# Optimization experiments

Measured on AMD Instinct MI355X. Metric: run time of the kernel, lower is better.

Reference implementation:

```python
import jax, jax.numpy as jnp
import numpy as np

B, V, NF, K = 16, 5000, 352, 120


def setup_inputs() -> dict:
    key = jax.random.key(0)
    k1, k2, k3, k4 = jax.random.split(key, 4)
    return {
        "feat_x": jax.random.normal(k1, (B, V, NF), dtype=jnp.float32),
        "feat_y": jax.random.normal(k2, (B, V, NF), dtype=jnp.float32),
        "evecs_x": jax.random.normal(k3, (B, V, K), dtype=jnp.float32),
        "evecs_y": jax.random.normal(k4, (B, V, K), dtype=jnp.float32),
    }


def reference(feat_x, feat_y, evecs_x, evecs_y):
    # Spectral coefficients: F_hat[b] = (evecs_x[b]^T feat_x[b])^T -> [B, F, K]
    F_hat = jnp.einsum("bvk,bvf->bfk", evecs_x, feat_x)
    G_hat = jnp.einsum("bvk,bvf->bfk", evecs_y, feat_y)

    # C1[b] = (inv(F^T F) F^T G)^T, batched least-squares solve
    FtF = jnp.einsum("bfk,bfl->bkl", F_hat, F_hat)  # [B,K,K]
    FtG = jnp.einsum("bfk,bfl->bkl", F_hat, G_hat)  # [B,K,K]
    C1 = jnp.linalg.solve(FtF, FtG).transpose(0, 2, 1)

    GtG = jnp.einsum("bfk,bfl->bkl", G_hat, G_hat)
    GtF = jnp.einsum("bfk,bfl->bkl", G_hat, F_hat)
    C2 = jnp.linalg.solve(GtG, GtF).transpose(0, 2, 1)
    return (C1, C2)
```

## Files before the change

### kernel.cpp

```cpp
#include <hip/hip_runtime.h>
#include <hip/hip_bf16.h>

#define NB 16
#define VV 5000
#define NFD 352
#define KD 120

typedef __attribute__((ext_vector_type(8))) short short8;
typedef __attribute__((ext_vector_type(4))) float float4v;

__device__ __forceinline__ void load_lds16(const float* g, float* l) {
    __builtin_amdgcn_global_load_lds(
        (const __attribute__((address_space(1))) unsigned int*)g,
        (__attribute__((address_space(3))) unsigned int*)l, 16, 0, 0);
}

__device__ __forceinline__ short bfbits(const __hip_bfloat16 h) {
    return (short)__builtin_bit_cast(unsigned short, h);
}

template <int STRIDE>
__device__ __forceinline__ void cvt_frag(const float* p, short8& hi, short8& lo) {
    #pragma unroll
    for (int j = 0; j < 8; ++j) {
        const float a = p[j * STRIDE];
        const __hip_bfloat16 h = __float2bfloat16(a);
        const float hf = __bfloat162float(h);
        const __hip_bfloat16 l = __float2bfloat16(a - hf);
        hi[j] = bfbits(h);
        lo[j] = bfbits(l);
    }
}

__global__ __launch_bounds__(256, 2) void proj_mfma(
    const float* __restrict__ fx, const float* __restrict__ fy,
    const float* __restrict__ ex, const float* __restrict__ ey,
    float* __restrict__ partials, const float* __restrict__ zeropad)
{
    const int t  = threadIdx.x;
    const int mt = blockIdx.x & 3;
    const int ch = blockIdx.x >> 2;
    const int wh = blockIdx.y;
    const int b  = blockIdx.z;

    const float* Ab = (wh ? fy : fx) + (size_t)b * VV * NFD;
    const float* Bb = (wh ? ey : ex) + (size_t)b * VV * KD;
    const int m0 = mt * 96;

    __shared__ float ldsA[64 * 96];
    __shared__ float ldsB[64 * 128];

    int akk[6]; const float* asrc0[6]; bool aok[6];
    #pragma unroll
    for (int i = 0; i < 6; ++i) {
        const int e  = i * 1024 + t * 4;
        const int k  = e / 96;
        const int c4 = (e - k * 96) >> 2;
        const int s  = ((k >> 3) & 3) << 1;
        const int mg = c4 ^ s;
        const int col = m0 + (mg << 2);
        akk[i] = k;
        aok[i] = (col < NFD);
        asrc0[i] = Ab + col;
    }
    int bkk[8]; const float* bsrc0[8]; bool bok[8];
    #pragma unroll
    for (int i = 0; i < 8; ++i) {
        const int e  = i * 1024 + t * 4;
        const int k  = e >> 7;
        const int c4 = (e >> 2) & 31;
        const int s  = ((k >> 3) & 3) << 1;
        const int ng = c4 ^ s;
        const int col = ng << 2;
        bkk[i] = k;
        bok[i] = (col < KD);
        bsrc0[i] = Bb + col;
    }

    const int wid = t >> 6;
    const int lane = t & 63;
    const int wm = wid >> 1, wn = wid & 1;
    const int row16 = lane & 15;
    const int g = lane >> 4;
    const int sl = (g & 3) << 1;

    int aidx[3];
    #pragma unroll
    for (int mf = 0; mf < 3; ++mf) {
        const int m = wm * 48 + mf * 16 + row16;
        aidx[mf] = (g * 8) * 96 + ((((m >> 2) ^ sl)) << 2) + (m & 3);
    }
    int bidx[4];
    #pragma unroll
    for (int nf = 0; nf < 4; ++nf) {
        const int n = wn * 64 + nf * 16 + row16;
        bidx[nf] = (g * 8) * 128 + ((((n >> 2) ^ sl)) << 2) + (n & 3);
    }

    float4v acc[3][4];
    #pragma unroll
    for (int mf = 0; mf < 3; ++mf)
        #pragma unroll
        for (int nf = 0; nf < 4; ++nf)
            acc[mf][nf] = float4v{0.f, 0.f, 0.f, 0.f};

    const int step0  = ch * 20;
    const int nsteps = (ch < 3) ? 20 : 19;

    for (int st = 0; st < nsteps; ++st) {
        const int v0 = (step0 + st) * 64;

        #pragma unroll
        for (int i = 0; i < 6; ++i) {
            const int v = v0 + akk[i];
            const float* src = (aok[i] && v < VV) ? (asrc0[i] + (size_t)v * NFD) : zeropad;
            load_lds16(src, &ldsA[i * 1024 + t * 4]);
        }
        #pragma unroll
        for (int i = 0; i < 8; ++i) {
            const int v = v0 + bkk[i];
            const float* src = (bok[i] && v < VV) ? (bsrc0[i] + (size_t)v * KD) : zeropad;
            load_lds16(src, &ldsB[i * 1024 + t * 4]);
        }
        __syncthreads();

        #pragma unroll
        for (int ks = 0; ks < 2; ++ks) {
            short8 ah[3], al[3], bh[4], bl[4];
            #pragma unroll
            for (int mf = 0; mf < 3; ++mf)
                cvt_frag<96>(&ldsA[ks * 32 * 96 + aidx[mf]], ah[mf], al[mf]);
            #pragma unroll
            for (int nf = 0; nf < 4; ++nf)
                cvt_frag<128>(&ldsB[ks * 32 * 128 + bidx[nf]], bh[nf], bl[nf]);

            #pragma unroll
            for (int mf = 0; mf < 3; ++mf)
                #pragma unroll
                for (int nf = 0; nf < 4; ++nf) {
                    acc[mf][nf] = __builtin_amdgcn_mfma_f32_16x16x32_bf16(ah[mf], bh[nf], acc[mf][nf], 0, 0, 0);
                    acc[mf][nf] = __builtin_amdgcn_mfma_f32_16x16x32_bf16(ah[mf], bl[nf], acc[mf][nf], 0, 0, 0);
                    acc[mf][nf] = __builtin_amdgcn_mfma_f32_16x16x32_bf16(al[mf], bh[nf], acc[mf][nf], 0, 0, 0);
                }
        }
        __syncthreads();
    }

    float* slab = partials + (size_t)((ch * 2 + wh) * NB + b) * (352 * 128);
    #pragma unroll
    for (int mf = 0; mf < 3; ++mf) {
        const int mrow = mt * 96 + wm * 48 + mf * 16 + g * 4;
        #pragma unroll
        for (int nf = 0; nf < 4; ++nf) {
            const int n = wn * 64 + nf * 16 + row16;
            #pragma unroll
            for (int r = 0; r < 4; ++r) {
                const int m = mrow + r;
                if (m < NFD) slab[(size_t)m * 128 + n] = acc[mf][nf][r];
            }
        }
    }
}

__global__ __launch_bounds__(256) void reduce_k(
    const float* __restrict__ partials, float* __restrict__ fhat, float* __restrict__ ghat)
{
    const int id = blockIdx.x * 256 + threadIdx.x;
    if (id >= NFD * KD) return;
    const int wb = blockIdx.y;
    const int wh = wb >> 4;
    const int b  = wb & 15;
    const int f = id / KD;
    const int k = id - f * KD;

    const size_t slabsz = 352 * 128;
    const float* p = partials + (size_t)(wh * NB + b) * slabsz + (size_t)f * 128 + k;
    const size_t chstride = (size_t)2 * NB * slabsz;

    float s = 0.f;
    #pragma unroll
    for (int c = 0; c < 4; ++c) s += p[c * chstride];

    float* dst = (wh ? ghat : fhat) + (size_t)b * NFD * KD + id;
    *dst = s;
}

__device__ __forceinline__ void gemm_tn_64x64(
    const float* __restrict__ A, const float* __restrict__ B, float* __restrict__ C,
    int V, int M, int N, int m0, int n0)
{
    __shared__ float As[16][64];
    __shared__ float Bs[16][64];

    const int tid = threadIdx.x;
    const int tx = tid & 15;
    const int ty = tid >> 4;
    const int sr = tid >> 4;
    const int sc = (tid & 15) << 2;

    float acc[4][4] = {{0.f,0.f,0.f,0.f},{0.f,0.f,0.f,0.f},
                       {0.f,0.f,0.f,0.f},{0.f,0.f,0.f,0.f}};

    for (int v0 = 0; v0 < V; v0 += 16) {
        const int v = v0 + sr;
        float4 av; av.x = av.y = av.z = av.w = 0.f;
        float4 bv; bv.x = bv.y = bv.z = bv.w = 0.f;
        if (v < V) {
            const float* Ar = A + (size_t)v * M;
            const int ca = m0 + sc;
            if (ca + 3 < M) {
                av = *(const float4*)(Ar + ca);
            } else {
                if (ca + 0 < M) av.x = Ar[ca + 0];
                if (ca + 1 < M) av.y = Ar[ca + 1];
                if (ca + 2 < M) av.z = Ar[ca + 2];
                if (ca + 3 < M) av.w = Ar[ca + 3];
            }
            const float* Br = B + (size_t)v * N;
            const int cb = n0 + sc;
            if (cb + 3 < N) {
                bv = *(const float4*)(Br + cb);
            } else {
                if (cb + 0 < N) bv.x = Br[cb + 0];
                if (cb + 1 < N) bv.y = Br[cb + 1];
                if (cb + 2 < N) bv.z = Br[cb + 2];
                if (cb + 3 < N) bv.w = Br[cb + 3];
            }
        }
        __syncthreads();
        *(float4*)&As[sr][sc] = av;
        *(float4*)&Bs[sr][sc] = bv;
        __syncthreads();

        #pragma unroll
        for (int kk = 0; kk < 16; ++kk) {
            const float4 a4 = *(const float4*)&As[kk][ty << 2];
            const float4 b4 = *(const float4*)&Bs[kk][tx << 2];
            const float a[4]  = {a4.x, a4.y, a4.z, a4.w};
            const float bb[4] = {b4.x, b4.y, b4.z, b4.w};
            #pragma unroll
            for (int i = 0; i < 4; ++i)
                #pragma unroll
                for (int j = 0; j < 4; ++j)
                    acc[i][j] = fmaf(a[i], bb[j], acc[i][j]);
        }
    }

    #pragma unroll
    for (int i = 0; i < 4; ++i) {
        const int m = m0 + (ty << 2) + i;
        if (m < M) {
            #pragma unroll
            for (int j = 0; j < 4; ++j) {
                const int n = n0 + (tx << 2) + j;
                if (n < N) C[(size_t)m * N + n] = acc[i][j];
            }
        }
    }
}

__global__ __launch_bounds__(256) void gram_kernel(
    const float* __restrict__ fhat, const float* __restrict__ ghat,
    float* __restrict__ ftf, float* __restrict__ gtg, float* __restrict__ ftg)
{
    const int b = blockIdx.z;
    const int which = blockIdx.y;
    const int m0 = (blockIdx.x & 1) * 64;
    const int n0 = (blockIdx.x >> 1) * 64;

    const float* F = fhat + (size_t)b * NFD * KD;
    const float* G = ghat + (size_t)b * NFD * KD;
    const float* A  = (which == 1) ? G : F;
    const float* Bp = (which == 0) ? F : G;
    float* C = ((which == 0) ? ftf : (which == 1) ? gtg : ftg) + (size_t)b * KD * KD;

    gemm_tn_64x64(A, Bp, C, NFD, KD, KD, m0, n0);
}

__device__ __forceinline__ float ldval(const float* __restrict__ A, const float* __restrict__ B,
                                       int pair, int row, int col) {
    if (col < KD) return A[row * KD + col];
    const int l = col - KD;
    return pair ? B[l * KD + row] : B[row * KD + l];
}

#define FOR30(OP) OP(0) OP(1) OP(2) OP(3) OP(4) OP(5) OP(6) OP(7) OP(8) OP(9) \
                  OP(10) OP(11) OP(12) OP(13) OP(14) OP(15) OP(16) OP(17) OP(18) OP(19) \
                  OP(20) OP(21) OP(22) OP(23) OP(24) OP(25) OP(26) OP(27) OP(28) OP(29)

__global__ __launch_bounds__(960, 1) void solve_kernel(
    const float* __restrict__ ftf, const float* __restrict__ gtg,
    const float* __restrict__ ftg, float* __restrict__ out)
{
    const int pair = blockIdx.x;
    const int b = blockIdx.y;
    const int tid = threadIdx.x;
    const int row   = tid >> 3;
    const int cg    = tid & 7;
    const int cbase = cg * 30;

    const float* Ag = ((pair == 0) ? ftf : gtg) + (size_t)b * KD * KD;
    const float* Bg = ftg + (size_t)b * KD * KD;

    __shared__ float prow[2][240];
    __shared__ float pcol[2][120];

    #define DECLC(I) float c##I = ldval(Ag, Bg, pair, row, cbase + (I));
    FOR30(DECLC)
    #undef DECLC

    if (row == 0) {
        #define PUBR0(I) prow[0][cbase + (I)] = c##I;
        FOR30(PUBR0)
        #undef PUBR0
    }
    if (cg == 0) pcol[0][row] = c0;
    __syncthreads();

    for (int j = 0; j < KD; ++j) {
        const int cur = j & 1;
        const int nxt = cur ^ 1;

        const float pinv = 1.0f / prow[cur][j];

        #define PRS(I) const float p##I = prow[cur][cbase + (I)] * pinv;
        FOR30(PRS)
        #undef PRS

        const float f = pcol[cur][row];

        #define UPDC(I) c##I = fmaf(-f, p##I, c##I);
        FOR30(UPDC)
        #undef UPDC

        if (row == j) {
            #define FIXC(I) c##I = p##I;
            FOR30(FIXC)
            #undef FIXC
        }

        const int j2 = j + 1;
        if (row == j2) {
            #define PUBR(I) prow[nxt][cbase + (I)] = c##I;
            FOR30(PUBR)
            #undef PUBR
        }
        if (j2 < KD && cg == (j2 / 30)) {
            #define PCASE(I) case I: pcol[nxt][row] = c##I; break;
            switch (j2 - cbase) {
                FOR30(PCASE)
                default: break;
            }
            #undef PCASE
        }
        __syncthreads();
    }

    float* op = out + (size_t)pair * NB * KD * KD + (size_t)b * KD * KD;
    if (cg >= 4) {
        #define OUTW(I) { const int l = cbase + (I) - KD; op[l * KD + row] = c##I; }
        FOR30(OUTW)
        #undef OUTW
    }
}

extern "C" void kernel_launch(void* const* d_in, const int* in_sizes, int n_in,
                              void* d_out, int out_size, void* d_ws, size_t ws_size,
                              hipStream_t stream)
{
    const float* feat_x  = (const float*)d_in[0];
    const float* feat_y  = (const float*)d_in[1];
    const float* evecs_x = (const float*)d_in[2];
    const float* evecs_y = (const float*)d_in[3];
    float* out = (float*)d_out;

    float* ws       = (float*)d_ws;
    float* zeropad  = ws;
    float* partials = ws + 64;
    float* fhat     = partials + (size_t)4 * 2 * NB * 352 * 128;
    float* ghat     = fhat + (size_t)NB * NFD * KD;
    float* ftf      = ghat + (size_t)NB * NFD * KD;
    float* gtg      = ftf  + (size_t)NB * KD * KD;
    float* ftg      = gtg  + (size_t)NB * KD * KD;

    hipMemsetAsync(zeropad, 0, 256, stream);

    proj_mfma <<<dim3(16, 2, NB), 256, 0, stream>>>(feat_x, feat_y, evecs_x, evecs_y, partials, zeropad);
    reduce_k  <<<dim3(165, 32), 256, 0, stream>>>(partials, fhat, ghat);
    gram_kernel<<<dim3(4, 3, NB), 256, 0, stream>>>(fhat, ghat, ftf, gtg, ftg);
    solve_kernel<<<dim3(2, NB), 960, 0, stream>>>(ftf, gtg, ftg, out);
}
```

Baseline: 250.0 us.

## Register-prefetch projection tiles, pre-split bf16 in LDS, vectorize solve row access

The projection GEMM drops the direct global-to-LDS loads. Each thread now loads into registers, splits the values into bf16 hi/lo once, and stores them swizzled in LDS, with the next tile's loads overlapping the MFMA work on the current tile. The tile grows to 128x128 over 5 V-chunks, and partials are stored compactly with stride 120 so the zero-pad buffer and memset go away. The solve kernel reads and writes pivot rows as float4 and folds pinv into one scalar multiplier. This trades more registers and a larger padded tile (wasted M/N work) for fewer LDS conversions and hidden load latency.

```diff
diff --git a/kernel.cpp b/kernel.cpp
--- a/kernel.cpp
+++ b/kernel.cpp
@@ -5,137 +5,175 @@
 #define VV 5000
 #define NFD 352
 #define KD 120
+#define NCH 5
+#define SLABSZ (352 * 120)
 
 typedef __attribute__((ext_vector_type(8))) short short8;
 typedef __attribute__((ext_vector_type(4))) float float4v;
 
-__device__ __forceinline__ void load_lds16(const float* g, float* l) {
-    __builtin_amdgcn_global_load_lds(
-        (const __attribute__((address_space(1))) unsigned int*)g,
-        (__attribute__((address_space(3))) unsigned int*)l, 16, 0, 0);
-}
-
-__device__ __forceinline__ short bfbits(const __hip_bfloat16 h) {
-    return (short)__builtin_bit_cast(unsigned short, h);
-}
-
-template <int STRIDE>
-__device__ __forceinline__ void cvt_frag(const float* p, short8& hi, short8& lo) {
+__device__ __forceinline__ unsigned short bfb(float a) {
+    return __builtin_bit_cast(unsigned short, __float2bfloat16(a));
+}
+
+__device__ __forceinline__ void pack8(const float* f, int4& hi, int4& lo) {
+    unsigned short h[8], l[8];
     #pragma unroll
     for (int j = 0; j < 8; ++j) {
-        const float a = p[j * STRIDE];
-        const __hip_bfloat16 h = __float2bfloat16(a);
-        const float hf = __bfloat162float(h);
-        const __hip_bfloat16 l = __float2bfloat16(a - hf);
-        hi[j] = bfbits(h);
-        lo[j] = bfbits(l);
-    }
+        const float a = f[j];
+        const __hip_bfloat16 hb = __float2bfloat16(a);
+        h[j] = __builtin_bit_cast(unsigned short, hb);
+        l[j] = bfb(a - __bfloat162float(hb));
+    }
+    hi.x = h[0] | (h[1] << 16); hi.y = h[2] | (h[3] << 16);
+    hi.z = h[4] | (h[5] << 16); hi.w = h[6] | (h[7] << 16);
+    lo.x = l[0] | (l[1] << 16); lo.y = l[2] | (l[3] << 16);
+    lo.z = l[4] | (l[5] << 16); lo.w = l[6] | (l[7] << 16);
 }
 
 __global__ __launch_bounds__(256, 2) void proj_mfma(
     const float* __restrict__ fx, const float* __restrict__ fy,
     const float* __restrict__ ex, const float* __restrict__ ey,
-    float* __restrict__ partials, const float* __restrict__ zeropad)
+    float* __restrict__ partials)
 {
     const int t  = threadIdx.x;
-    const int mt = blockIdx.x & 3;
-    const int ch = blockIdx.x >> 2;
+    const int mt = blockIdx.x % 3;
+    const int ch = blockIdx.x / 3;
     const int wh = blockIdx.y;
     const int b  = blockIdx.z;
 
     const float* Ab = (wh ? fy : fx) + (size_t)b * VV * NFD;
     const float* Bb = (wh ? ey : ex) + (size_t)b * VV * KD;
-    const int m0 = mt * 96;
-
-    __shared__ float ldsA[64 * 96];
-    __shared__ float ldsB[64 * 128];
-
-    int akk[6]; const float* asrc0[6]; bool aok[6];
-    #pragma unroll
-    for (int i = 0; i < 6; ++i) {
-        const int e  = i * 1024 + t * 4;
-        const int k  = e / 96;
-        const int c4 = (e - k * 96) >> 2;
-        const int s  = ((k >> 3) & 3) << 1;
-        const int mg = c4 ^ s;
-        const int col = m0 + (mg << 2);
-        akk[i] = k;
-        aok[i] = (col < NFD);
-        asrc0[i] = Ab + col;
-    }
-    int bkk[8]; const float* bsrc0[8]; bool bok[8];
-    #pragma unroll
-    for (int i = 0; i < 8; ++i) {
-        const int e  = i * 1024 + t * 4;
-        const int k  = e >> 7;
-        const int c4 = (e >> 2) & 31;
-        const int s  = ((k >> 3) & 3) << 1;
-        const int ng = c4 ^ s;
-        const int col = ng << 2;
-        bkk[i] = k;
-        bok[i] = (col < KD);
-        bsrc0[i] = Bb + col;
-    }
-
-    const int wid = t >> 6;
+    const int m0 = mt * 128;
+
+    __shared__ int4 smem4[4096];
+    unsigned char* smem = (unsigned char*)smem4;
+
+    int aoff[4], awb[4], ao[4];
+    #pragma unroll
+    for (int i = 0; i < 4; ++i) {
+        const int q = i * 256 + t;
+        const int m = q & 127;
+        const int o = q >> 7;
+        const int col = min(m0 + m, NFD - 1);
+        aoff[i] = col + o * 8 * NFD;
+        awb[i]  = m * 128 + ((o ^ (m & 7)) * 16);
+        ao[i]   = o;
+    }
+    int boff[4], bwb[4], bo[4];
+    #pragma unroll
+    for (int i = 0; i < 4; ++i) {
+        const int q = i * 256 + t;
+        const int n = q & 127;
+        const int o = q >> 7;
+        const int col = min(n, KD - 1);
+        boff[i] = col + o * 8 * KD;
+        bwb[i]  = 32768 + n * 128 + ((o ^ (n & 7)) * 16);
+        bo[i]   = o;
+    }
+
     const int lane = t & 63;
+    const int wid  = t >> 6;
     const int wm = wid >> 1, wn = wid & 1;
-    const int row16 = lane & 15;
-    const int g = lane >> 4;
-    const int sl = (g & 3) << 1;
-
-    int aidx[3];
-    #pragma unroll
-    for (int mf = 0; mf < 3; ++mf) {
-        const int m = wm * 48 + mf * 16 + row16;
-        aidx[mf] = (g * 8) * 96 + ((((m >> 2) ^ sl)) << 2) + (m & 3);
-    }
-    int bidx[4];
+    const int r16 = lane & 15;
+    const int g   = lane >> 4;
+
+    int abase[4], bbase[4];
+    #pragma unroll
+    for (int mf = 0; mf < 4; ++mf) {
+        const int m = wm * 64 + mf * 16 + r16;
+        abase[mf] = m * 128 + ((g ^ (m & 7)) * 16);
+    }
     #pragma unroll
     for (int nf = 0; nf < 4; ++nf) {
-        const int n = wn * 64 + nf * 16 + row16;
-        bidx[nf] = (g * 8) * 128 + ((((n >> 2) ^ sl)) << 2) + (n & 3);
-    }
-
-    float4v acc[3][4];
-    #pragma unroll
-    for (int mf = 0; mf < 3; ++mf)
+        const int n = wn * 64 + nf * 16 + r16;
+        bbase[nf] = 32768 + n * 128 + ((g ^ (n & 7)) * 16);
+    }
+
+    float4v acc[4][4];
+    #pragma unroll
+    for (int mf = 0; mf < 4; ++mf)
         #pragma unroll
         for (int nf = 0; nf < 4; ++nf)
             acc[mf][nf] = float4v{0.f, 0.f, 0.f, 0.f};
 
-    const int step0  = ch * 20;
-    const int nsteps = (ch < 3) ? 20 : 19;
-
-    for (int st = 0; st < nsteps; ++st) {
-        const int v0 = (step0 + st) * 64;
-
-        #pragma unroll
-        for (int i = 0; i < 6; ++i) {
-            const int v = v0 + akk[i];
-            const float* src = (aok[i] && v < VV) ? (asrc0[i] + (size_t)v * NFD) : zeropad;
-            load_lds16(src, &ldsA[i * 1024 + t * 4]);
-        }
-        #pragma unroll
-        for (int i = 0; i < 8; ++i) {
-            const int v = v0 + bkk[i];
-            const float* src = (bok[i] && v < VV) ? (bsrc0[i] + (size_t)v * KD) : zeropad;
-            load_lds16(src, &ldsB[i * 1024 + t * 4]);
-        }
-        __syncthreads();
+    const int step0 = ch * 16;
+    const int nst   = (ch < 4) ? 16 : 15;
+
+    float fa[4][8], fb[4][8];
+
+    auto do_loads = [&](int v0) {
+        const int va = v0 * NFD;
+        const int vb = v0 * KD;
+        if (v0 + 64 <= VV) {
+            #pragma unroll
+            for (int i = 0; i < 4; ++i)
+                #pragma unroll
+                for (int j = 0; j < 8; ++j)
+                    fa[i][j] = Ab[aoff[i] + va + j * NFD];
+            #pragma unroll
+            for (int i = 0; i < 4; ++i)
+                #pragma unroll
+                for (int j = 0; j < 8; ++j)
+                    fb[i][j] = Bb[boff[i] + vb + j * KD];
+        } else {
+            #pragma unroll
+            for (int i = 0; i < 4; ++i)
+                #pragma unroll
+                for (int j = 0; j < 8; ++j) {
+                    const int v = v0 + ao[i] * 8 + j;
+                    fa[i][j] = (v < VV) ? Ab[aoff[i] + va + j * NFD] : 0.f;
+                }
+            #pragma unroll
+            for (int i = 0; i < 4; ++i)
+                #pragma unroll
+                for (int j = 0; j < 8; ++j) {
+                    const int v = v0 + bo[i] * 8 + j;
+                    fb[i][j] = (v < VV) ? Bb[boff[i] + vb + j * KD] : 0.f;
+                }
+        }
+    };
+    auto do_writes = [&]() {
+        #pragma unroll
+        for (int i = 0; i < 4; ++i) {
+            int4 hi, lo;
+            pack8(fa[i], hi, lo);
+            *(int4*)(smem + awb[i])         = hi;
+            *(int4*)(smem + awb[i] + 16384) = lo;
+        }
+        #pragma unroll
+        for (int i = 0; i < 4; ++i) {
+            int4 hi, lo;
+            pack8(fb[i], hi, lo);
+            *(int4*)(smem + bwb[i])         = hi;
+            *(int4*)(smem + bwb[i] + 16384) = lo;
+        }
+    };
+
+    do_loads(step0 * 64);
+    do_writes();
+    __syncthreads();
+
+    for (int st = 0; st < nst; ++st) {
+        const bool more = (st + 1 < nst);
+        if (more) do_loads((step0 + st + 1) * 64);
 
         #pragma unroll
         for (int ks = 0; ks < 2; ++ks) {
-            short8 ah[3], al[3], bh[4], bl[4];
-            #pragma unroll
-            for (int mf = 0; mf < 3; ++mf)
-                cvt_frag<96>(&ldsA[ks * 32 * 96 + aidx[mf]], ah[mf], al[mf]);
-            #pragma unroll
-            for (int nf = 0; nf < 4; ++nf)
-                cvt_frag<128>(&ldsB[ks * 32 * 128 + bidx[nf]], bh[nf], bl[nf]);
-
-            #pragma unroll
-            for (int mf = 0; mf < 3; ++mf)
+            short8 ah[4], al[4], bh[4], bl[4];
+            #pragma unroll
+            for (int mf = 0; mf < 4; ++mf) {
+                const int ad = abase[mf] ^ (ks * 64);
+                ah[mf] = *(const short8*)(smem + ad);
+                al[mf] = *(const short8*)(smem + ad + 16384);
+            }
+            #pragma unroll
+            for (int nf = 0; nf < 4; ++nf) {
+                const int bd = bbase[nf] ^ (ks * 64);
+                bh[nf] = *(const short8*)(smem + bd);
+                bl[nf] = *(const short8*)(smem + bd + 16384);
+            }
+            #pragma unroll
+            for (int mf = 0; mf < 4; ++mf)
                 #pragma unroll
                 for (int nf = 0; nf < 4; ++nf) {
                     acc[mf][nf] = __builtin_amdgcn_mfma_f32_16x16x32_bf16(ah[mf], bh[nf], acc[mf][nf], 0, 0, 0);
@@ -144,19 +182,25 @@
                 }
         }
         __syncthreads();
-    }
-
-    float* slab = partials + (size_t)((ch * 2 + wh) * NB + b) * (352 * 128);
-    #pragma unroll
-    for (int mf = 0; mf < 3; ++mf) {
-        const int mrow = mt * 96 + wm * 48 + mf * 16 + g * 4;
+        if (more) {
+            do_writes();
+            __syncthreads();
+        }
+    }
+
+    float* slab = partials + (size_t)((ch * 2 + wh) * NB + b) * SLABSZ;
+    #pragma unroll
+    for (int mf = 0; mf < 4; ++mf) {
+        const int mrow = mt * 128 + wm * 64 + mf * 16 + g * 4;
         #pragma unroll
         for (int nf = 0; nf < 4; ++nf) {
-            const int n = wn * 64 + nf * 16 + row16;
-            #pragma unroll
-            for (int r = 0; r < 4; ++r) {
-                const int m = mrow + r;
-                if (m < NFD) slab[(size_t)m * 128 + n] = acc[mf][nf][r];
+            const int n = wn * 64 + nf * 16 + r16;
+            if (n < KD) {
+                #pragma unroll
+                for (int r = 0; r < 4; ++r) {
+                    const int m = mrow + r;
+                    if (m < NFD) slab[(size_t)m * KD + n] = acc[mf][nf][r];
+                }
             }
         }
     }
@@ -170,16 +214,13 @@
     const int wb = blockIdx.y;
     const int wh = wb >> 4;
     const int b  = wb & 15;
-    const int f = id / KD;
-    const int k = id - f * KD;
-
-    const size_t slabsz = 352 * 128;
-    const float* p = partials + (size_t)(wh * NB + b) * slabsz + (size_t)f * 128 + k;
-    const size_t chstride = (size_t)2 * NB * slabsz;
+
+    const float* p = partials + (size_t)(wh * NB + b) * SLABSZ + id;
+    const size_t chstride = (size_t)2 * NB * SLABSZ;
 
     float s = 0.f;
     #pragma unroll
-    for (int c = 0; c < 4; ++c) s += p[c * chstride];
+    for (int c = 0; c < NCH; ++c) s += p[c * chstride];
 
     float* dst = (wh ? ghat : fhat) + (size_t)b * NFD * KD + id;
     *dst = s;
@@ -298,11 +339,12 @@
     const int row   = tid >> 3;
     const int cg    = tid & 7;
     const int cbase = cg * 30;
+    const int seg   = cg * 32;
 
     const float* Ag = ((pair == 0) ? ftf : gtg) + (size_t)b * KD * KD;
     const float* Bg = ftg + (size_t)b * KD * KD;
 
-    __shared__ float prow[2][240];
+    __shared__ __align__(16) float prow[2][256];
     __shared__ float pcol[2][120];
 
     #define DECLC(I) float c##I = ldval(Ag, Bg, pair, row, cbase + (I));
@@ -310,47 +352,83 @@
     #undef DECLC
 
     if (row == 0) {
-        #define PUBR0(I) prow[0][cbase + (I)] = c##I;
-        FOR30(PUBR0)
-        #undef PUBR0
+        float4 w;
+        w = float4{c0,c1,c2,c3};     *(float4*)&prow[0][seg + 0]  = w;
+        w = float4{c4,c5,c6,c7};     *(float4*)&prow[0][seg + 4]  = w;
+        w = float4{c8,c9,c10,c11};   *(float4*)&prow[0][seg + 8]  = w;
+        w = float4{c12,c13,c14,c15}; *(float4*)&prow[0][seg + 12] = w;
+        w = float4{c16,c17,c18,c19}; *(float4*)&prow[0][seg + 16] = w;
+        w = float4{c20,c21,c22,c23}; *(float4*)&prow[0][seg + 20] = w;
+        w = float4{c24,c25,c26,c27}; *(float4*)&prow[0][seg + 24] = w;
+        *(float2*)&prow[0][seg + 28] = float2{c28, c29};
     }
     if (cg == 0) pcol[0][row] = c0;
     __syncthreads();
+
+    int iseg = 0, ioff = 0;
 
     for (int j = 0; j < KD; ++j) {
         const int cur = j & 1;
         const int nxt = cur ^ 1;
 
-        const float pinv = 1.0f / prow[cur][j];
-
-        #define PRS(I) const float p##I = prow[cur][cbase + (I)] * pinv;
-        FOR30(PRS)
-        #undef PRS
-
-        const float f = pcol[cur][row];
-
-        #define UPDC(I) c##I = fmaf(-f, p##I, c##I);
-        FOR30(UPDC)
-        #undef UPDC
+        const float pv   = prow[cur][(iseg << 5) + ioff];
+        const float pinv = 1.0f / pv;
+        const float f    = pcol[cur][row];
+        const float fp   = f * pinv;
+
+        const float4 r0 = *(const float4*)&prow[cur][seg + 0];
+        const float4 r1 = *(const float4*)&prow[cur][seg + 4];
+        const float4 r2 = *(const float4*)&prow[cur][seg + 8];
+        const float4 r3 = *(const float4*)&prow[cur][seg + 12];
+        const float4 r4 = *(const float4*)&prow[cur][seg + 16];
+        const float4 r5 = *(const float4*)&prow[cur][seg + 20];
+        const float4 r6 = *(const float4*)&prow[cur][seg + 24];
+        const float2 r7 = *(const float2*)&prow[cur][seg + 28];
+
+        c0  = fmaf(-fp, r0.x, c0);  c1  = fmaf(-fp, r0.y, c1);
+        c2  = fmaf(-fp, r0.z, c2);  c3  = fmaf(-fp, r0.w, c3);
+        c4  = fmaf(-fp, r1.x, c4);  c5  = fmaf(-fp, r1.y, c5);
+        c6  = fmaf(-fp, r1.z, c6);  c7  = fmaf(-fp, r1.w, c7);
+        c8  = fmaf(-fp, r2.x, c8);  c9  = fmaf(-fp, r2.y, c9);
+        c10 = fmaf(-fp, r2.z, c10); c11 = fmaf(-fp, r2.w, c11);
+        c12 = fmaf(-fp, r3.x, c12); c13 = fmaf(-fp, r3.y, c13);
+        c14 = fmaf(-fp, r3.z, c14); c15 = fmaf(-fp, r3.w, c15);
+        c16 = fmaf(-fp, r4.x, c16); c17 = fmaf(-fp, r4.y, c17);
+        c18 = fmaf(-fp, r4.z, c18); c19 = fmaf(-fp, r4.w, c19);
+        c20 = fmaf(-fp, r5.x, c20); c21 = fmaf(-fp, r5.y, c21);
+        c22 = fmaf(-fp, r5.z, c22); c23 = fmaf(-fp, r5.w, c23);
+        c24 = fmaf(-fp, r6.x, c24); c25 = fmaf(-fp, r6.y, c25);
+        c26 = fmaf(-fp, r6.z, c26); c27 = fmaf(-fp, r6.w, c27);
+        c28 = fmaf(-fp, r7.x, c28); c29 = fmaf(-fp, r7.y, c29);
 
         if (row == j) {
-            #define FIXC(I) c##I = p##I;
-            FOR30(FIXC)
-            #undef FIXC
+            c0  = r0.x * pinv; c1  = r0.y * pinv; c2  = r0.z * pinv; c3  = r0.w * pinv;
+            c4  = r1.x * pinv; c5  = r1.y * pinv; c6  = r1.z * pinv; c7  = r1.w * pinv;
+            c8  = r2.x * pinv; c9  = r2.y * pinv; c10 = r2.z * pinv; c11 = r2.w * pinv;
+            c12 = r3.x * pinv; c13 = r3.y * pinv; c14 = r3.z * pinv; c15 = r3.w * pinv;
+            c16 = r4.x * pinv; c17 = r4.y * pinv; c18 = r4.z * pinv; c19 = r4.w * pinv;
+            c20 = r5.x * pinv; c21 = r5.y * pinv; c22 = r5.z * pinv; c23 = r5.w * pinv;
+            c24 = r6.x * pinv; c25 = r6.y * pinv; c26 = r6.z * pinv; c27 = r6.w * pinv;
+            c28 = r7.x * pinv; c29 = r7.y * pinv;
         }
 
         const int j2 = j + 1;
         if (row == j2) {
-            #define PUBR(I) prow[nxt][cbase + (I)] = c##I;
-            FOR30(PUBR)
-            #undef PUBR
-        }
-        if (j2 < KD && cg == (j2 / 30)) {
+            float4 w;
+            w = float4{c0,c1,c2,c3};     *(float4*)&prow[nxt][seg + 0]  = w;
+            w = float4{c4,c5,c6,c7};     *(float4*)&prow[nxt][seg + 4]  = w;
+            w = float4{c8,c9,c10,c11};   *(float4*)&prow[nxt][seg + 8]  = w;
+            w = float4{c12,c13,c14,c15}; *(float4*)&prow[nxt][seg + 12] = w;
+            w = float4{c16,c17,c18,c19}; *(float4*)&prow[nxt][seg + 16] = w;
+            w = float4{c20,c21,c22,c23}; *(float4*)&prow[nxt][seg + 20] = w;
+            w = float4{c24,c25,c26,c27}; *(float4*)&prow[nxt][seg + 24] = w;
+            *(float2*)&prow[nxt][seg + 28] = float2{c28, c29};
+        }
+
+        ioff++; if (ioff == 30) { ioff = 0; iseg++; }
+        if (j2 < KD && cg == iseg) {
             #define PCASE(I) case I: pcol[nxt][row] = c##I; break;
-            switch (j2 - cbase) {
-                FOR30(PCASE)
-                default: break;
-            }
+            switch (ioff) { FOR30(PCASE) default: break; }
             #undef PCASE
         }
         __syncthreads();
@@ -375,17 +453,14 @@
     float* out = (float*)d_out;
 
     float* ws       = (float*)d_ws;
-    float* zeropad  = ws;
-    float* partials = ws + 64;
-    float* fhat     = partials + (size_t)4 * 2 * NB * 352 * 128;
+    float* partials = ws;
+    float* fhat     = partials + (size_t)NCH * 2 * NB * SLABSZ;
     float* ghat     = fhat + (size_t)NB * NFD * KD;
-    float* ftf      = ghat + (size_t)NB * NFD * KD;
-    float* gtg      = ftf  + (size_t)NB * KD * KD;
-    float* ftg      = gtg  + (size_t)NB * KD * KD;
-
-    hipMemsetAsync(zeropad, 0, 256, stream);
-
-    proj_mfma <<<dim3(16, 2, NB), 256, 0, stream>>>(feat_x, feat_y, evecs_x, evecs_y, partials, zeropad);
+    float* ftf      = ws;
+    float* gtg      = ftf + (size_t)NB * KD * KD;
+    float* ftg      = gtg + (size_t)NB * KD * KD;
+
+    proj_mfma <<<dim3(15, 2, NB), 256, 0, stream>>>(feat_x, feat_y, evecs_x, evecs_y, partials);
     reduce_k  <<<dim3(165, 32), 256, 0, stream>>>(partials, fhat, ghat);
     gram_kernel<<<dim3(4, 3, NB), 256, 0, stream>>>(fhat, ghat, ftf, gtg, ftg);
     solve_kernel<<<dim3(2, NB), 960, 0, stream>>>(ftf, gtg, ftg, out);
```

New measurement: 262.2 us. 1.05x slower.
